# Kernel tuning notes

Hardware: AMD Instinct MI355X
Metric: run time of the kernel (lower is better)

The kernel has to match this reference:

```python
import jax, jax.numpy as jnp
import numpy as np

DIM = 384
HEADS = 12
CUBE = (4, 7, 7)
N = CUBE[0] * CUBE[1] * CUBE[2]  # 196
HIDDEN = 4 * DIM
BW = 256  # num_windows * batch
EPS = 1e-5


def _relative_position_index():
    c, h, w = CUBE
    coords = np.stack(np.meshgrid(np.arange(c), np.arange(h), np.arange(w), indexing='ij'))  # [3,c,h,w]
    flat = coords.reshape(3, -1)  # [3, N]
    rel = flat[:, :, None] - flat[:, None, :]  # [3, N, N]
    rel = rel.transpose(1, 2, 0).copy()
    rel[:, :, 0] += c - 1
    rel[:, :, 1] += h - 1
    rel[:, :, 2] += w - 1
    rel[:, :, 1] *= 2 * w - 1
    rel[:, :, 0] *= (2 * h - 1) * (2 * w - 1)
    return rel.sum(-1).astype(np.int32)  # [N, N]


def setup_inputs() -> dict:
    key = jax.random.key(0)
    ks = jax.random.split(key, 16)
    s = 0.02
    table_rows = (2 * CUBE[0] - 1) * (2 * CUBE[1] - 1) * (2 * CUBE[2] - 1)
    return {
        'x': jax.random.normal(ks[0], (BW, N, DIM), jnp.float32),
        'norm1_w': jnp.ones((DIM,), jnp.float32),
        'norm1_b': jnp.zeros((DIM,), jnp.float32),
        'qkv_w': jax.random.normal(ks[1], (DIM, 3 * DIM), jnp.float32) * s,
        'qkv_b': jnp.zeros((3 * DIM,), jnp.float32),
        'proj_w': jax.random.normal(ks[2], (DIM, DIM), jnp.float32) * s,
        'proj_b': jnp.zeros((DIM,), jnp.float32),
        'rpb_table': jax.random.normal(ks[3], (table_rows, HEADS), jnp.float32) * s,
        'norm2_w': jnp.ones((DIM,), jnp.float32),
        'norm2_b': jnp.zeros((DIM,), jnp.float32),
        'fc1_w': jax.random.normal(ks[4], (DIM, HIDDEN), jnp.float32) * s,
        'fc1_b': jnp.zeros((HIDDEN,), jnp.float32),
        'fc2_w': jax.random.normal(ks[5], (HIDDEN, DIM), jnp.float32) * s,
        'fc2_b': jnp.zeros((DIM,), jnp.float32),
        'rpi': jnp.asarray(_relative_position_index()),
    }


def _layernorm(x, w, b):
    mu = jnp.mean(x, axis=-1, keepdims=True)
    var = jnp.mean(jnp.square(x - mu), axis=-1, keepdims=True)
    return (x - mu) * jax.lax.rsqrt(var + EPS) * w + b


def reference(x, norm1_w, norm1_b, qkv_w, qkv_b, proj_w, proj_b, rpb_table,
              norm2_w, norm2_b, fc1_w, fc1_b, fc2_w, fc2_b, rpi):
    B_, n, C = x.shape
    hd = C // HEADS
    scale = hd ** (-0.5)

    # --- attention branch ---
    h = _layernorm(x, norm1_w, norm1_b)
    qkv = (h @ qkv_w + qkv_b).reshape(B_, n, 3, HEADS, hd)
    q, k, v = qkv[:, :, 0], qkv[:, :, 1], qkv[:, :, 2]  # [B_, n, H, hd]
    attn = jnp.einsum('bqhd,bkhd->bhqk', q * scale, k)
    bias = rpb_table[rpi]                 # [n, n, H]
    attn = attn + jnp.transpose(bias, (2, 0, 1))[None]
    attn = jax.nn.softmax(attn, axis=-1)
    out = jnp.einsum('bhqk,bkhd->bqhd', attn, v).reshape(B_, n, C)
    out = out @ proj_w + proj_b
    x = x + out

    # --- MLP branch ---
    h = _layernorm(x, norm2_w, norm2_b)
    h = jax.nn.gelu(h @ fc1_w + fc1_b, approximate=False)
    h = h @ fc2_w + fc2_b
    return x + h
```

## Files before the change

### kernel.cpp

```cpp
#include <hip/hip_runtime.h>
#include <hip/hip_bf16.h>
#include <math.h>

#define NDIM 384
#define NHEADS 12
#define NTOK 196
#define NBATCH 256
#define M_TOK (NBATCH * NTOK)
#define NHID 1536
#define THREE_DIM 1152
#define HD 32
#define EPSV 1e-5f

typedef __hip_bfloat16 bf16;
typedef __attribute__((ext_vector_type(8))) short short8;
typedef __attribute__((ext_vector_type(4))) float f32x4;

__device__ __forceinline__ void gload_lds16(const void* g, void* l) {
  __builtin_amdgcn_global_load_lds((const __attribute__((address_space(1))) void*)g,
                                   (__attribute__((address_space(3))) void*)l, 16, 0, 0);
}

__global__ void k_transpose_bf16(const float* __restrict__ src, bf16* __restrict__ dst,
                                 int K, int N) {
  int idx = blockIdx.x * 256 + threadIdx.x;
  if (idx >= K * N) return;
  int k = idx / N, n = idx - k * N;
  dst[n * K + k] = __float2bfloat16(src[idx]);
}

__global__ void k_build_bias(const float* __restrict__ table, const int* __restrict__ rpi,
                             float* __restrict__ bias_mat) {
  int idx = blockIdx.x * 256 + threadIdx.x;
  if (idx >= NTOK * NTOK) return;
  int r = rpi[idx];
#pragma unroll
  for (int h = 0; h < NHEADS; ++h)
    bias_mat[h * (NTOK * NTOK) + idx] = table[r * NHEADS + h];
}

__global__ __launch_bounds__(256) void k_layernorm(const float* __restrict__ x,
                                                   const float* __restrict__ w,
                                                   const float* __restrict__ b,
                                                   bf16* __restrict__ out) {
  int token = blockIdx.x * 4 + (threadIdx.x >> 6);
  int lane = threadIdx.x & 63;
  const float* xr = x + (size_t)token * NDIM;
  float v[6];
  float s = 0.f;
#pragma unroll
  for (int i = 0; i < 6; ++i) { v[i] = xr[lane + i * 64]; s += v[i]; }
#pragma unroll
  for (int off = 32; off >= 1; off >>= 1) s += __shfl_xor(s, off);
  float mu = s * (1.f / NDIM);
  float s2 = 0.f;
#pragma unroll
  for (int i = 0; i < 6; ++i) { float d = v[i] - mu; s2 += d * d; }
#pragma unroll
  for (int off = 32; off >= 1; off >>= 1) s2 += __shfl_xor(s2, off);
  float r = rsqrtf(s2 * (1.f / NDIM) + EPSV);
  bf16* orow = out + (size_t)token * NDIM;
#pragma unroll
  for (int i = 0; i < 6; ++i) {
    int c = lane + i * 64;
    orow[c] = __float2bfloat16((v[i] - mu) * r * w[c] + b[c]);
  }
}

template <int EPI>
__global__ __launch_bounds__(256) void k_gemm_bt(const bf16* __restrict__ A,
                                                 const bf16* __restrict__ Bt,
                                                 const float* __restrict__ bias,
                                                 const float* __restrict__ resid,
                                                 void* __restrict__ Cout,
                                                 int Nn, int K, int nbx) {
  __shared__ bf16 As[2][128 * 32];
  __shared__ bf16 Bs[2][128 * 32];
  const int tid = threadIdx.x;
  const int wave = tid >> 6, lane = tid & 63;
  const int lo = lane & 15, hi = lane >> 4;
  const int wm = wave >> 1, wn = wave & 1;

  const int nwg = gridDim.x;
  const int swz = (blockIdx.x & 7) * (nwg >> 3) + (blockIdx.x >> 3);
  const int m0 = (swz / nbx) * 128, n0 = (swz % nbx) * 128;

  f32x4 acc[4][4];
#pragma unroll
  for (int i = 0; i < 4; ++i) {
#pragma unroll
    for (int j = 0; j < 4; ++j) acc[i][j] = (f32x4){0.f, 0.f, 0.f, 0.f};
  }

  const int row = tid >> 2, part = tid & 3;
  const int row1 = (256 + tid) >> 2, part1 = tid & 3;

  gload_lds16(A + (size_t)(m0 + row) * K + part * 8, As[0] + tid * 8);
  gload_lds16(Bt + (size_t)(n0 + row) * K + part * 8, Bs[0] + tid * 8);
  gload_lds16(A + (size_t)(m0 + row1) * K + part1 * 8, As[0] + (256 + tid) * 8);
  gload_lds16(Bt + (size_t)(n0 + row1) * K + part1 * 8, Bs[0] + (256 + tid) * 8);
  __syncthreads();

  const int nk = K >> 5;
  int cur = 0;
  for (int ks = 0; ks < nk; ++ks) {
    if (ks + 1 < nk) {
      int k0 = (ks + 1) << 5;
      gload_lds16(A + (size_t)(m0 + row) * K + k0 + part * 8, As[cur ^ 1] + tid * 8);
      gload_lds16(Bt + (size_t)(n0 + row) * K + k0 + part * 8, Bs[cur ^ 1] + tid * 8);
      gload_lds16(A + (size_t)(m0 + row1) * K + k0 + part1 * 8, As[cur ^ 1] + (256 + tid) * 8);
      gload_lds16(Bt + (size_t)(n0 + row1) * K + k0 + part1 * 8, Bs[cur ^ 1] + (256 + tid) * 8);
    }
    short8 af[4], bfr[4];
#pragma unroll
    for (int i = 0; i < 4; ++i) {
      af[i] = *(const short8*)(As[cur] + (wm * 64 + i * 16 + lo) * 32 + hi * 8);
      bfr[i] = *(const short8*)(Bs[cur] + (wn * 64 + i * 16 + lo) * 32 + hi * 8);
    }
#pragma unroll
    for (int i = 0; i < 4; ++i) {
#pragma unroll
      for (int j = 0; j < 4; ++j)
        acc[i][j] = __builtin_amdgcn_mfma_f32_16x16x32_bf16(af[i], bfr[j], acc[i][j], 0, 0, 0);
    }
    __syncthreads();
    cur ^= 1;
  }

#pragma unroll
  for (int i = 0; i < 4; ++i) {
    int r = m0 + wm * 64 + i * 16 + hi * 4;
#pragma unroll
    for (int j = 0; j < 4; ++j) {
      int cb = n0 + wn * 64 + j * 16 + lo;
      float bv = bias[cb];
#pragma unroll
      for (int e = 0; e < 4; ++e) {
        size_t idx = (size_t)(r + e) * Nn + cb;
        float val = acc[i][j][e] + bv;
        if (EPI == 1) val = 0.5f * val * (1.f + erff(val * 0.70710678118f));
        if (EPI == 2) {
          ((float*)Cout)[idx] = resid[idx] + val;
        } else {
          ((bf16*)Cout)[idx] = __float2bfloat16(val);
        }
      }
    }
  }
}

__global__ __launch_bounds__(256) void k_attn(const bf16* __restrict__ qkv,
                                              const float* __restrict__ bias_mat,
                                              bf16* __restrict__ out) {
  __shared__ __align__(16) bf16 Vt[32][232];
  __shared__ __align__(16) bf16 Ps[4][16][232];
  const int tid = threadIdx.x;
  const int wave = tid >> 6, lane = tid & 63;
  const int lo = lane & 15, hi = lane >> 4;
  const int h = blockIdx.x;
  const int b = blockIdx.y;
  const float scale = 0.17677669529663687f;
  const bf16* Kbase = qkv + (size_t)b * NTOK * THREE_DIM + NDIM + h * HD;
  const bf16* Vbase = qkv + (size_t)b * NTOK * THREE_DIM + 2 * NDIM + h * HD;
  const bf16* Qbase = qkv + (size_t)b * NTOK * THREE_DIM + h * HD;

  union U8 { short8 v; bf16 x[8]; };
  for (int u = tid; u < NTOK * 4; u += 256) {
    int t = u >> 2, dseg = (u & 3) * 8;
    U8 vv;
    vv.v = *(const short8*)(Vbase + (size_t)t * THREE_DIM + dseg);
#pragma unroll
    for (int j = 0; j < 8; ++j) Vt[dseg + j][t] = vv.x[j];
  }
  for (int u = tid; u < 32 * 28; u += 256) {
    int d = u / 28, c = 196 + u % 28;
    Vt[d][c] = __float2bfloat16(0.f);
  }
  for (int i = lane; i < 16 * 16; i += 64) {
    Ps[wave][i >> 4][208 + (i & 15)] = __float2bfloat16(0.f);
  }
  __syncthreads();

  for (int qt = wave; qt < 13; qt += 4) {
    int qrow = qt * 16 + lo;
    short8 qf = {0, 0, 0, 0, 0, 0, 0, 0};
    if (qrow < NTOK) qf = *(const short8*)(Qbase + (size_t)qrow * THREE_DIM + hi * 8);

    f32x4 s[13];
#pragma unroll
    for (int kt = 0; kt < 13; ++kt) {
      int key = kt * 16 + lo;
      short8 kf = {0, 0, 0, 0, 0, 0, 0, 0};
      if (key < NTOK) kf = *(const short8*)(Kbase + (size_t)key * THREE_DIM + hi * 8);
      f32x4 z = {0.f, 0.f, 0.f, 0.f};
      s[kt] = __builtin_amdgcn_mfma_f32_16x16x32_bf16(qf, kf, z, 0, 0, 0);
    }

#pragma unroll
    for (int e = 0; e < 4; ++e) {
      int qg = qt * 16 + hi * 4 + e;
      int qc = qg < NTOK ? qg : NTOK - 1;
      const float* brow = bias_mat + ((size_t)h * NTOK + qc) * NTOK;
      float mx = -1e30f;
#pragma unroll
      for (int kt = 0; kt < 13; ++kt) {
        int key = kt * 16 + lo;
        float v = (key < NTOK) ? (s[kt][e] * scale + brow[key]) : -1e30f;
        s[kt][e] = v;
        mx = fmaxf(mx, v);
      }
#pragma unroll
      for (int off = 8; off >= 1; off >>= 1) mx = fmaxf(mx, __shfl_xor(mx, off));
      float sm = 0.f;
#pragma unroll
      for (int kt = 0; kt < 13; ++kt) {
        float pe = __expf(s[kt][e] - mx);
        s[kt][e] = pe;
        sm += pe;
      }
#pragma unroll
      for (int off = 8; off >= 1; off >>= 1) sm += __shfl_xor(sm, off);
      float inv = 1.f / sm;
#pragma unroll
      for (int kt = 0; kt < 13; ++kt) s[kt][e] *= inv;
    }

#pragma unroll
    for (int kt = 0; kt < 13; ++kt) {
#pragma unroll
      for (int e = 0; e < 4; ++e)
        Ps[wave][hi * 4 + e][kt * 16 + lo] = __float2bfloat16(s[kt][e]);
    }

    f32x4 o[2] = {{0.f, 0.f, 0.f, 0.f}, {0.f, 0.f, 0.f, 0.f}};
#pragma unroll
    for (int c = 0; c < 7; ++c) {
      short8 pa = *(const short8*)(&Ps[wave][lo][c * 32 + hi * 8]);
#pragma unroll
      for (int n = 0; n < 2; ++n) {
        short8 vf = *(const short8*)(&Vt[n * 16 + lo][c * 32 + hi * 8]);
        o[n] = __builtin_amdgcn_mfma_f32_16x16x32_bf16(pa, vf, o[n], 0, 0, 0);
      }
    }

#pragma unroll
    for (int n = 0; n < 2; ++n) {
#pragma unroll
      for (int e = 0; e < 4; ++e) {
        int qg = qt * 16 + hi * 4 + e;
        if (qg < NTOK)
          out[(size_t)(b * NTOK + qg) * NDIM + h * HD + n * 16 + lo] = __float2bfloat16(o[n][e]);
      }
    }
  }
}

extern "C" void kernel_launch(void* const* d_in, const int* in_sizes, int n_in,
                              void* d_out, int out_size, void* d_ws, size_t ws_size,
                              hipStream_t stream) {
  const float* x       = (const float*)d_in[0];
  const float* norm1_w = (const float*)d_in[1];
  const float* norm1_b = (const float*)d_in[2];
  const float* qkv_w   = (const float*)d_in[3];
  const float* qkv_b   = (const float*)d_in[4];
  const float* proj_w  = (const float*)d_in[5];
  const float* proj_b  = (const float*)d_in[6];
  const float* rpb     = (const float*)d_in[7];
  const float* norm2_w = (const float*)d_in[8];
  const float* norm2_b = (const float*)d_in[9];
  const float* fc1_w   = (const float*)d_in[10];
  const float* fc1_b   = (const float*)d_in[11];
  const float* fc2_w   = (const float*)d_in[12];
  const float* fc2_b   = (const float*)d_in[13];
  const int*   rpi     = (const int*)d_in[14];
  float* out = (float*)d_out;

  char* ws = (char*)d_ws;
  bf16* qkv_buf = (bf16*)ws;
  bf16* mlp1 = (bf16*)ws;
  bf16* hbuf = (bf16*)(ws + 154140672);
  bf16* wqkv_t = (bf16*)(ws + 154140672 + 38535168);
  bf16* wproj_t = wqkv_t + 442368;
  bf16* wfc1_t = wproj_t + 147456;
  bf16* wfc2_t = wfc1_t + 589824;
  float* bias_mat = (float*)(wfc2_t + 589824);

  k_transpose_bf16<<<(442368 + 255) / 256, 256, 0, stream>>>(qkv_w, wqkv_t, 384, 1152);
  k_transpose_bf16<<<(147456 + 255) / 256, 256, 0, stream>>>(proj_w, wproj_t, 384, 384);
  k_transpose_bf16<<<(589824 + 255) / 256, 256, 0, stream>>>(fc1_w, wfc1_t, 384, 1536);
  k_transpose_bf16<<<(589824 + 255) / 256, 256, 0, stream>>>(fc2_w, wfc2_t, 1536, 384);
  k_build_bias<<<(NTOK * NTOK + 255) / 256, 256, 0, stream>>>(rpb, rpi, bias_mat);

  k_layernorm<<<M_TOK / 4, 256, 0, stream>>>(x, norm1_w, norm1_b, hbuf);
  k_gemm_bt<0><<<9 * 392, 256, 0, stream>>>(hbuf, wqkv_t, qkv_b, nullptr, qkv_buf, 1152, 384, 9);
  k_attn<<<dim3(NHEADS, NBATCH), 256, 0, stream>>>(qkv_buf, bias_mat, hbuf);
  k_gemm_bt<2><<<3 * 392, 256, 0, stream>>>(hbuf, wproj_t, proj_b, x, out, 384, 384, 3);
  k_layernorm<<<M_TOK / 4, 256, 0, stream>>>(out, norm2_w, norm2_b, hbuf);
  k_gemm_bt<1><<<12 * 392, 256, 0, stream>>>(hbuf, wfc1_t, fc1_b, nullptr, mlp1, 1536, 384, 12);
  k_gemm_bt<2><<<3 * 392, 256, 0, stream>>>(mlp1, wfc2_t, fc2_b, out, out, 384, 1536, 3);
}
```

Baseline: 544.2 us.

## Scatter QKV into padded per-head buffers and run one wave per query tile

The QKV GEMM epilogue now writes Q and K into padded per-(batch, head) tiles and V pre-transposed, instead of one interleaved row-major buffer. This removes the LDS transpose and block-wide sync in the attention kernel. The attention kernel now gives each wave its own independent 16-query tile and raises wave priority around the MFMA sections. In exchange, the GEMM epilogue does scattered, poorly coalesced stores, especially for transposed V, and V is re-read from global memory by every wave. The padded token slots are never initialised, so the code relies on masking and zero probabilities to neutralise whatever is left in the workspace.

```diff
diff --git a/kernel.cpp b/kernel.cpp
--- a/kernel.cpp
+++ b/kernel.cpp
@@ -11,6 +11,7 @@
 #define THREE_DIM 1152
 #define HD 32
 #define EPSV 1e-5f
+#define BH_STRIDE 7168
 
 typedef __hip_bfloat16 bf16;
 typedef __attribute__((ext_vector_type(8))) short short8;
@@ -73,6 +74,9 @@
                                                  const float* __restrict__ bias,
                                                  const float* __restrict__ resid,
                                                  void* __restrict__ Cout,
+                                                 bf16* __restrict__ pq,
+                                                 bf16* __restrict__ pk,
+                                                 bf16* __restrict__ pv,
                                                  int Nn, int K, int nbx) {
   __shared__ bf16 As[2][128 * 32];
   __shared__ bf16 Bs[2][128 * 32];
@@ -129,19 +133,33 @@
 
 #pragma unroll
   for (int i = 0; i < 4; ++i) {
-    int r = m0 + wm * 64 + i * 16 + hi * 4;
+    int rbase = m0 + wm * 64 + i * 16 + hi * 4;
 #pragma unroll
     for (int j = 0; j < 4; ++j) {
       int cb = n0 + wn * 64 + j * 16 + lo;
       float bv = bias[cb];
 #pragma unroll
       for (int e = 0; e < 4; ++e) {
-        size_t idx = (size_t)(r + e) * Nn + cb;
+        int rr = rbase + e;
         float val = acc[i][j][e] + bv;
         if (EPI == 1) val = 0.5f * val * (1.f + erff(val * 0.70710678118f));
         if (EPI == 2) {
+          size_t idx = (size_t)rr * Nn + cb;
           ((float*)Cout)[idx] = resid[idx] + val;
+        } else if (EPI == 3) {
+          int d = cb & 31;
+          int hseg = cb >> 5;
+          int which = hseg / 12;
+          int h = hseg - which * 12;
+          int b = rr / 196;
+          int t = rr - b * 196;
+          size_t base = (size_t)(b * 12 + h) * BH_STRIDE;
+          bf16 v16 = __float2bfloat16(val);
+          if (which == 2) pv[base + d * 224 + t] = v16;
+          else if (which == 1) pk[base + t * 32 + d] = v16;
+          else pq[base + t * 32 + d] = v16;
         } else {
+          size_t idx = (size_t)rr * Nn + cb;
           ((bf16*)Cout)[idx] = __float2bfloat16(val);
         }
       }
@@ -149,108 +167,96 @@
   }
 }
 
-__global__ __launch_bounds__(256) void k_attn(const bf16* __restrict__ qkv,
+__global__ __launch_bounds__(256) void k_attn(const bf16* __restrict__ Qp,
+                                              const bf16* __restrict__ Kp,
+                                              const bf16* __restrict__ Vtp,
                                               const float* __restrict__ bias_mat,
                                               bf16* __restrict__ out) {
-  __shared__ __align__(16) bf16 Vt[32][232];
   __shared__ __align__(16) bf16 Ps[4][16][232];
   const int tid = threadIdx.x;
   const int wave = tid >> 6, lane = tid & 63;
   const int lo = lane & 15, hi = lane >> 4;
-  const int h = blockIdx.x;
-  const int b = blockIdx.y;
+  const int unit = blockIdx.x * 4 + wave;
+  const int bh = unit / 13;
+  const int qt = unit - bh * 13;
+  const int h = bh % 12;
+  const int b = bh / 12;
   const float scale = 0.17677669529663687f;
-  const bf16* Kbase = qkv + (size_t)b * NTOK * THREE_DIM + NDIM + h * HD;
-  const bf16* Vbase = qkv + (size_t)b * NTOK * THREE_DIM + 2 * NDIM + h * HD;
-  const bf16* Qbase = qkv + (size_t)b * NTOK * THREE_DIM + h * HD;
-
-  union U8 { short8 v; bf16 x[8]; };
-  for (int u = tid; u < NTOK * 4; u += 256) {
-    int t = u >> 2, dseg = (u & 3) * 8;
-    U8 vv;
-    vv.v = *(const short8*)(Vbase + (size_t)t * THREE_DIM + dseg);
-#pragma unroll
-    for (int j = 0; j < 8; ++j) Vt[dseg + j][t] = vv.x[j];
-  }
-  for (int u = tid; u < 32 * 28; u += 256) {
-    int d = u / 28, c = 196 + u % 28;
-    Vt[d][c] = __float2bfloat16(0.f);
-  }
-  for (int i = lane; i < 16 * 16; i += 64) {
+  const bf16* Qb = Qp + (size_t)bh * BH_STRIDE;
+  const bf16* Kb = Kp + (size_t)bh * BH_STRIDE;
+  const bf16* Vb = Vtp + (size_t)bh * BH_STRIDE;
+
+  for (int i = lane; i < 256; i += 64)
     Ps[wave][i >> 4][208 + (i & 15)] = __float2bfloat16(0.f);
-  }
-  __syncthreads();
-
-  for (int qt = wave; qt < 13; qt += 4) {
-    int qrow = qt * 16 + lo;
-    short8 qf = {0, 0, 0, 0, 0, 0, 0, 0};
-    if (qrow < NTOK) qf = *(const short8*)(Qbase + (size_t)qrow * THREE_DIM + hi * 8);
-
-    f32x4 s[13];
+
+  short8 qf = *(const short8*)(Qb + (qt * 16 + lo) * 32 + hi * 8);
+
+  f32x4 s[13];
+  __builtin_amdgcn_s_setprio(1);
+#pragma unroll
+  for (int kt = 0; kt < 13; ++kt) {
+    short8 kf = *(const short8*)(Kb + (kt * 16 + lo) * 32 + hi * 8);
+    f32x4 z = {0.f, 0.f, 0.f, 0.f};
+    s[kt] = __builtin_amdgcn_mfma_f32_16x16x32_bf16(qf, kf, z, 0, 0, 0);
+  }
+  __builtin_amdgcn_s_setprio(0);
+
+#pragma unroll
+  for (int e = 0; e < 4; ++e) {
+    int qg = qt * 16 + hi * 4 + e;
+    int qc = qg < NTOK ? qg : NTOK - 1;
+    const float* brow = bias_mat + ((size_t)h * NTOK + qc) * NTOK;
+    float mx = -1e30f;
 #pragma unroll
     for (int kt = 0; kt < 13; ++kt) {
       int key = kt * 16 + lo;
-      short8 kf = {0, 0, 0, 0, 0, 0, 0, 0};
-      if (key < NTOK) kf = *(const short8*)(Kbase + (size_t)key * THREE_DIM + hi * 8);
-      f32x4 z = {0.f, 0.f, 0.f, 0.f};
-      s[kt] = __builtin_amdgcn_mfma_f32_16x16x32_bf16(qf, kf, z, 0, 0, 0);
-    }
-
+      float v = (key < NTOK) ? (s[kt][e] * scale + brow[key]) : -1e30f;
+      s[kt][e] = v;
+      mx = fmaxf(mx, v);
+    }
+#pragma unroll
+    for (int off = 8; off >= 1; off >>= 1) mx = fmaxf(mx, __shfl_xor(mx, off));
+    float sm = 0.f;
+#pragma unroll
+    for (int kt = 0; kt < 13; ++kt) {
+      float pe = __expf(s[kt][e] - mx);
+      s[kt][e] = pe;
+      sm += pe;
+    }
+#pragma unroll
+    for (int off = 8; off >= 1; off >>= 1) sm += __shfl_xor(sm, off);
+    float inv = 1.f / sm;
+#pragma unroll
+    for (int kt = 0; kt < 13; ++kt) s[kt][e] *= inv;
+  }
+
+#pragma unroll
+  for (int kt = 0; kt < 13; ++kt) {
+#pragma unroll
+    for (int e = 0; e < 4; ++e)
+      Ps[wave][hi * 4 + e][kt * 16 + lo] = __float2bfloat16(s[kt][e]);
+  }
+
+  f32x4 o[2] = {{0.f, 0.f, 0.f, 0.f}, {0.f, 0.f, 0.f, 0.f}};
+  __builtin_amdgcn_s_setprio(1);
+#pragma unroll
+  for (int c = 0; c < 7; ++c) {
+    short8 pa = *(const short8*)(&Ps[wave][lo][c * 32 + hi * 8]);
+#pragma unroll
+    for (int n = 0; n < 2; ++n) {
+      short8 vf = *(const short8*)(Vb + (n * 16 + lo) * 224 + c * 32 + hi * 8);
+      o[n] = __builtin_amdgcn_mfma_f32_16x16x32_bf16(pa, vf, o[n], 0, 0, 0);
+    }
+  }
+  __builtin_amdgcn_s_setprio(0);
+
+#pragma unroll
+  for (int n = 0; n < 2; ++n) {
 #pragma unroll
     for (int e = 0; e < 4; ++e) {
       int qg = qt * 16 + hi * 4 + e;
-      int qc = qg < NTOK ? qg : NTOK - 1;
-      const float* brow = bias_mat + ((size_t)h * NTOK + qc) * NTOK;
-      float mx = -1e30f;
-#pragma unroll
-      for (int kt = 0; kt < 13; ++kt) {
-        int key = kt * 16 + lo;
-        float v = (key < NTOK) ? (s[kt][e] * scale + brow[key]) : -1e30f;
-        s[kt][e] = v;
-        mx = fmaxf(mx, v);
-      }
-#pragma unroll
-      for (int off = 8; off >= 1; off >>= 1) mx = fmaxf(mx, __shfl_xor(mx, off));
-      float sm = 0.f;
-#pragma unroll
-      for (int kt = 0; kt < 13; ++kt) {
-        float pe = __expf(s[kt][e] - mx);
-        s[kt][e] = pe;
-        sm += pe;
-      }
-#pragma unroll
-      for (int off = 8; off >= 1; off >>= 1) sm += __shfl_xor(sm, off);
-      float inv = 1.f / sm;
-#pragma unroll
-      for (int kt = 0; kt < 13; ++kt) s[kt][e] *= inv;
-    }
-
-#pragma unroll
-    for (int kt = 0; kt < 13; ++kt) {
-#pragma unroll
-      for (int e = 0; e < 4; ++e)
-        Ps[wave][hi * 4 + e][kt * 16 + lo] = __float2bfloat16(s[kt][e]);
-    }
-
-    f32x4 o[2] = {{0.f, 0.f, 0.f, 0.f}, {0.f, 0.f, 0.f, 0.f}};
-#pragma unroll
-    for (int c = 0; c < 7; ++c) {
-      short8 pa = *(const short8*)(&Ps[wave][lo][c * 32 + hi * 8]);
-#pragma unroll
-      for (int n = 0; n < 2; ++n) {
-        short8 vf = *(const short8*)(&Vt[n * 16 + lo][c * 32 + hi * 8]);
-        o[n] = __builtin_amdgcn_mfma_f32_16x16x32_bf16(pa, vf, o[n], 0, 0, 0);
-      }
-    }
-
-#pragma unroll
-    for (int n = 0; n < 2; ++n) {
-#pragma unroll
-      for (int e = 0; e < 4; ++e) {
-        int qg = qt * 16 + hi * 4 + e;
-        if (qg < NTOK)
-          out[(size_t)(b * NTOK + qg) * NDIM + h * HD + n * 16 + lo] = __float2bfloat16(o[n][e]);
-      }
+      if (qg < NTOK)
+        out[(size_t)(b * NTOK + qg) * NDIM + h * HD + n * 16 + lo] = __float2bfloat16(o[n][e]);
     }
   }
 }
@@ -276,7 +282,9 @@
   float* out = (float*)d_out;
 
   char* ws = (char*)d_ws;
-  bf16* qkv_buf = (bf16*)ws;
+  bf16* pad_q = (bf16*)ws;
+  bf16* pad_k = (bf16*)(ws + 44040192);
+  bf16* pad_v = (bf16*)(ws + 2 * 44040192);
   bf16* mlp1 = (bf16*)ws;
   bf16* hbuf = (bf16*)(ws + 154140672);
   bf16* wqkv_t = (bf16*)(ws + 154140672 + 38535168);
@@ -292,10 +300,14 @@
   k_build_bias<<<(NTOK * NTOK + 255) / 256, 256, 0, stream>>>(rpb, rpi, bias_mat);
 
   k_layernorm<<<M_TOK / 4, 256, 0, stream>>>(x, norm1_w, norm1_b, hbuf);
-  k_gemm_bt<0><<<9 * 392, 256, 0, stream>>>(hbuf, wqkv_t, qkv_b, nullptr, qkv_buf, 1152, 384, 9);
-  k_attn<<<dim3(NHEADS, NBATCH), 256, 0, stream>>>(qkv_buf, bias_mat, hbuf);
-  k_gemm_bt<2><<<3 * 392, 256, 0, stream>>>(hbuf, wproj_t, proj_b, x, out, 384, 384, 3);
+  k_gemm_bt<3><<<9 * 392, 256, 0, stream>>>(hbuf, wqkv_t, qkv_b, nullptr, nullptr,
+                                            pad_q, pad_k, pad_v, 1152, 384, 9);
+  k_attn<<<9984, 256, 0, stream>>>(pad_q, pad_k, pad_v, bias_mat, hbuf);
+  k_gemm_bt<2><<<3 * 392, 256, 0, stream>>>(hbuf, wproj_t, proj_b, x, out,
+                                            nullptr, nullptr, nullptr, 384, 384, 3);
   k_layernorm<<<M_TOK / 4, 256, 0, stream>>>(out, norm2_w, norm2_b, hbuf);
-  k_gemm_bt<1><<<12 * 392, 256, 0, stream>>>(hbuf, wfc1_t, fc1_b, nullptr, mlp1, 1536, 384, 12);
-  k_gemm_bt<2><<<3 * 392, 256, 0, stream>>>(mlp1, wfc2_t, fc2_b, out, out, 384, 1536, 3);
-}
+  k_gemm_bt<1><<<12 * 392, 256, 0, stream>>>(hbuf, wfc1_t, fc1_b, nullptr, mlp1,
+                                             nullptr, nullptr, nullptr, 1536, 384, 12);
+  k_gemm_bt<2><<<3 * 392, 256, 0, stream>>>(mlp1, wfc2_t, fc2_b, out, out,
+                                            nullptr, nullptr, nullptr, 384, 1536, 3);
+}
```

Result: slower. 585.5 us (+7.6%).
